# Optimization experiments

Measured on AMD Instinct MI355X. Metric: run time of the kernel, lower is better.

## Reference

```python
import jax, jax.numpy as jnp
import numpy as np

OUT, IN, GROUP = 11008, 4096, 64
NUM_GROUPS = IN // GROUP  # pad = 0 since IN % GROUP == 0


def setup_inputs() -> dict:
    key = jax.random.key(0)
    k_x, k_q, k_s, k_b = jax.random.split(key, 4)
    x = jax.random.normal(k_x, (4, 2048, IN), dtype=jnp.float32)
    # int4 symmetric codes in [-8, 7], stored as int8 like the torch buffer
    qweight = jax.random.randint(k_q, (OUT, NUM_GROUPS, GROUP), -8, 8).astype(jnp.int8)
    # positive per-group scales (amax/7 in the original), stored fp16
    scales = (jax.random.uniform(k_s, (OUT, NUM_GROUPS), dtype=jnp.float32) * 0.02 + 1e-3).astype(jnp.float16)
    bias = (jax.random.normal(k_b, (OUT,), dtype=jnp.float32) * 0.02).astype(jnp.float16)
    return {"x": x, "qweight": qweight, "scales": scales, "bias": bias}


def reference(x, qweight, scales, bias):
    # Fused dequant: w[o, g*GROUP + j] = q[o, g, j] * scales[o, g]
    w = (qweight.astype(jnp.float16) * scales[:, :, None]).reshape(OUT, IN)
    w = w.astype(x.dtype)  # original casts dequantized weight to x.dtype
    # F.linear(x, w, bias): y = x @ w.T + b  -> [B, S, OUT]
    return jnp.einsum('bsi,oi->bso', x, w) + bias.astype(x.dtype)
```

## Files before the change

kernel.cpp:

```cpp
#include <hip/hip_runtime.h>
#include <hip/hip_fp16.h>
#include <stdint.h>


#define M_DIM 8192
#define N_DIM 11008
#define K_DIM 4096
#define MT_TILES 64
#define NT_TILES 43
#define K_TILES 128
#define SLAB 8192
#define RSTRIDE 12288

typedef short short8 __attribute__((ext_vector_type(8)));
typedef float floatx4 __attribute__((ext_vector_type(4)));

__device__ __forceinline__ unsigned short f2bf(float f) {
  union { float f; uint32_t u; } c; c.f = f;
  uint32_t u = c.u;
  return (unsigned short)((u + 0x7FFFu + ((u >> 16) & 1u)) >> 16);
}

__device__ __forceinline__ float load_sc(const void* p, size_t idx, bool is_f32) {
  if (is_f32) return ((const float*)p)[idx];
  return __half2float(((const __half*)p)[idx]);
}

__device__ __forceinline__ bool sniff_q_is_i32(const void* qv) {
  const int* w = (const int*)qv;
  bool ok = true;
  #pragma unroll
  for (int j = 0; j < 16; ++j) {
    int v = w[j];
    ok = ok && (v == (int)(signed char)(v & 0xFF));
  }
  return ok;
}
__device__ __forceinline__ bool sniff_s_is_f32(const void* sv) {
  const float* f = (const float*)sv;
  bool ok = true;
  #pragma unroll
  for (int j = 0; j < 8; ++j) {
    float v = f[j];
    ok = ok && (v > 4e-4f) && (v < 6e-2f);
  }
  return ok;
}

__device__ __forceinline__ void gload_lds16(const short* g, short* l) {
  __builtin_amdgcn_global_load_lds(
      (const __attribute__((address_space(1))) uint32_t*)g,
      (__attribute__((address_space(3))) uint32_t*)l, 16, 0, 0);
}

__global__ __launch_bounds__(256)
void prep_fused(const float* __restrict__ x, const void* __restrict__ qv,
                const void* __restrict__ sv,
                short* __restrict__ xh, short* __restrict__ wq) {
  const int tid = threadIdx.x;
  int b = blockIdx.x;

  if (b < NT_TILES * 256) {
    const bool q_is_i32 = sniff_q_is_i32(qv);
    const bool s_is_f32 = sniff_s_is_f32(sv);
    const int nt = b >> 8;
    const int rem = b & 255;
    const int kt = rem >> 1, half = rem & 1;
    const int r = half * 128 + (tid >> 1);
    const int s0 = (tid & 1) * 2;
    const int o = nt * 256 + r;
    const int k0 = kt * 32 + s0 * 8;

    const float s = load_sc(sv, (size_t)o * 64 + (kt >> 1), s_is_f32);

    int codes[16];
    if (q_is_i32) {
      const int* qq = (const int*)qv + (size_t)o * K_DIM + k0;
      #pragma unroll
      for (int j = 0; j < 4; ++j) {
        int4 t = ((const int4*)qq)[j];
        codes[j*4+0]=t.x; codes[j*4+1]=t.y; codes[j*4+2]=t.z; codes[j*4+3]=t.w;
      }
    } else {
      union { int4 v; int8_t c[16]; } u;
      u.v = *(const int4*)((const int8_t*)qv + (size_t)o * K_DIM + k0);
      #pragma unroll
      for (int j = 0; j < 16; ++j) codes[j] = (int)u.c[j];
    }

    short8 h0, h1;
    #pragma unroll
    for (int j = 0; j < 8; ++j) h0[j] = f2bf((float)codes[j] * s);
    #pragma unroll
    for (int j = 0; j < 8; ++j) h1[j] = f2bf((float)codes[8 + j] * s);

    const int w = (r >> 1) & 3;
    short* slab = wq + ((size_t)nt * K_TILES + kt) * SLAB;
    *(short8*)&slab[r * 32 + ((s0    ) ^ w) * 8] = h0;
    *(short8*)&slab[r * 32 + ((s0 + 1) ^ w) * 8] = h1;
  } else {
    b -= NT_TILES * 256;
    const int mt = b >> 8;
    const int rem = b & 255;
    const int kt = rem >> 1, half = rem & 1;
    const int r = half * 128 + (tid >> 1);
    const int s0 = (tid & 1) * 2;
    const int k0 = kt * 32 + s0 * 8;

    const float4* p = (const float4*)(x + (size_t)(mt * 256 + r) * K_DIM + k0);
    float4 f0 = p[0], f1 = p[1], f2 = p[2], f3 = p[3];
    short8 h0, h1;
    h0[0]=f2bf(f0.x); h0[1]=f2bf(f0.y); h0[2]=f2bf(f0.z); h0[3]=f2bf(f0.w);
    h0[4]=f2bf(f1.x); h0[5]=f2bf(f1.y); h0[6]=f2bf(f1.z); h0[7]=f2bf(f1.w);
    h1[0]=f2bf(f2.x); h1[1]=f2bf(f2.y); h1[2]=f2bf(f2.z); h1[3]=f2bf(f2.w);
    h1[4]=f2bf(f3.x); h1[5]=f2bf(f3.y); h1[6]=f2bf(f3.z); h1[7]=f2bf(f3.w);

    const int w = (r >> 1) & 3;
    short* slab = xh + ((size_t)mt * K_TILES + kt) * SLAB;
    *(short8*)&slab[r * 32 + ((s0    ) ^ w) * 8] = h0;
    *(short8*)&slab[r * 32 + ((s0 + 1) ^ w) * 8] = h1;
  }
}

__global__ __launch_bounds__(256, 2)
void gemm4(const short* __restrict__ xh, const short* __restrict__ wq,
           const void* __restrict__ sv, const void* __restrict__ bv,
           float* __restrict__ C) {
  __shared__ __align__(16) short lds[3 * RSTRIDE];

  const bool s_is_f32 = sniff_s_is_f32(sv);

  const int tid  = threadIdx.x;
  const int lane = tid & 63;
  const int wid  = tid >> 6;
  const int wm = wid >> 1, wn = wid & 1;
  const int lr = lane & 15, lk = lane >> 4;

  const int bid = blockIdx.x;
  const int xcd = bid & 7;
  const int seq = bid >> 3;
  const int nt  = seq >> 3;
  const int mt  = xcd * 8 + (seq & 7);

  const short* Aslab = xh + (size_t)(mt >> 1) * (K_TILES * SLAB) + (mt & 1) * 4096;
  const short* Bslab = wq + (size_t)nt * (K_TILES * SLAB);

  const int swz8 = (lk ^ ((lr >> 1) & 3)) << 3;
  int aoff[4], boff[8];
  #pragma unroll
  for (int mi = 0; mi < 4; ++mi) aoff[mi] = (wm * 64 + mi * 16 + lr) * 32 + swz8;
  #pragma unroll
  for (int ni = 0; ni < 8; ++ni) boff[ni] = (wn * 128 + ni * 16 + lr) * 32 + swz8;

  floatx4 acc[4][8];
  #pragma unroll
  for (int i = 0; i < 4; ++i)
    #pragma unroll
    for (int j = 0; j < 8; ++j)
      acc[i][j] = (floatx4){0.f, 0.f, 0.f, 0.f};

  short8 fa[4], fb[8], ga[4], gb[8];

#define SBAR __builtin_amdgcn_sched_barrier(0)
#define VMCNT(n) do { asm volatile("s_waitcnt vmcnt(" #n ")"); SBAR; } while (0)
#define LGKM0 do { asm volatile("s_waitcnt lgkmcnt(0)"); SBAR; } while (0)
#define BARRIER do { SBAR; __builtin_amdgcn_s_barrier(); SBAR; } while (0)

#define STAGE(t) do {                                                   \
    const int s_ = (t) % 3;                                             \
    const short* gA_ = Aslab + (size_t)(t) * SLAB;                      \
    const short* gB_ = Bslab + (size_t)(t) * SLAB;                      \
    short* lA_ = lds + s_ * RSTRIDE;                                    \
    short* lB_ = lA_ + 4096;                                            \
    gload_lds16(gA_ + tid * 8,        lA_ + tid * 8);                   \
    gload_lds16(gA_ + 2048 + tid * 8, lA_ + 2048 + tid * 8);            \
    gload_lds16(gB_ + tid * 8,        lB_ + tid * 8);                   \
    gload_lds16(gB_ + 2048 + tid * 8, lB_ + 2048 + tid * 8);            \
    gload_lds16(gB_ + 4096 + tid * 8, lB_ + 4096 + tid * 8);            \
    gload_lds16(gB_ + 6144 + tid * 8, lB_ + 6144 + tid * 8);            \
  } while (0)

#define LOADF(da, db, t) do {                                           \
    const short* lA_ = lds + ((t) % 3) * RSTRIDE;                       \
    const short* lB_ = lA_ + 4096;                                      \
    _Pragma("unroll")                                                   \
    for (int mi = 0; mi < 4; ++mi) da[mi] = *(const short8*)&lA_[aoff[mi]]; \
    _Pragma("unroll")                                                   \
    for (int ni = 0; ni < 8; ++ni) db[ni] = *(const short8*)&lB_[boff[ni]]; \
  } while (0)

#define DOMFMA(sa, sb) do {                                             \
    __builtin_amdgcn_s_setprio(1);                                      \
    _Pragma("unroll")                                                   \
    for (int mi = 0; mi < 4; ++mi)                                      \
      _Pragma("unroll")                                                 \
      for (int ni = 0; ni < 8; ++ni)                                    \
        acc[mi][ni] = __builtin_amdgcn_mfma_f32_16x16x32_bf16(          \
            sa[mi], sb[ni], acc[mi][ni], 0, 0, 0);                      \
    __builtin_amdgcn_s_setprio(0);                                      \
  } while (0)

  STAGE(0); STAGE(1); STAGE(2);
  VMCNT(12);
  BARRIER;
  LOADF(fa, fb, 0);

  for (int kt = 0; kt < 124; kt += 2) {
    VMCNT(6);
    LGKM0;
    BARRIER;
    STAGE(kt + 3);
    LOADF(ga, gb, kt + 1);
    DOMFMA(fa, fb);
    VMCNT(6);
    LGKM0;
    BARRIER;
    STAGE(kt + 4);
    LOADF(fa, fb, kt + 2);
    DOMFMA(ga, gb);
  }

  VMCNT(6);
  LGKM0;
  BARRIER;
  STAGE(127);
  LOADF(ga, gb, 125);
  DOMFMA(fa, fb);
  VMCNT(6);
  LGKM0;
  BARRIER;
  LOADF(fa, fb, 126);
  DOMFMA(ga, gb);
  VMCNT(0);
  LGKM0;
  BARRIER;
  LOADF(ga, gb, 127);
  DOMFMA(fa, fb);
  DOMFMA(ga, gb);

#undef STAGE
#undef LOADF
#undef DOMFMA
#undef SBAR
#undef VMCNT
#undef LGKM0
#undef BARRIER

  #pragma unroll
  for (int ni = 0; ni < 8; ++ni) {
    const int col = nt * 256 + wn * 128 + ni * 16 + lr;
    const float bvf = load_sc(bv, (size_t)col, s_is_f32);
    #pragma unroll
    for (int mi = 0; mi < 4; ++mi) {
      const int rbase = mt * 128 + wm * 64 + mi * 16 + lk * 4;
      #pragma unroll
      for (int rr = 0; rr < 4; ++rr)
        C[(size_t)(rbase + rr) * N_DIM + col] = acc[mi][ni][rr] + bvf;
    }
  }
}

__global__ __launch_bounds__(256)
void gemm_fused(const float* __restrict__ x, const void* __restrict__ qv,
                const void* __restrict__ sv, const void* __restrict__ bv,
                float* __restrict__ C) {
  __shared__ __align__(16) short As[128 * 64];
  __shared__ __align__(16) short Bs[128 * 64];

  const bool q_is_i32 = sniff_q_is_i32(qv);
  const bool s_is_f32 = sniff_s_is_f32(sv);

  const int tid  = threadIdx.x;
  const int lane = tid & 63;
  const int wid  = tid >> 6;
  const int wm = wid >> 1, wn = wid & 1;
  const int lr = lane & 15, lk = lane >> 4;

  const int nwg = gridDim.x;
  const int cpx = nwg >> 3;
  const int bid = blockIdx.x;
  const int swz = (bid & 7) * cpx + (bid >> 3);
  const int per_g = 4 * 86;
  const int g = swz / per_g;
  const int r = swz - g * per_g;
  const int mt = (g << 2) + (r & 3);
  const int nt = r >> 2;

  const int row0 = mt * 128;
  const int col0 = nt * 128;

  floatx4 acc[4][4];
  #pragma unroll
  for (int i = 0; i < 4; ++i)
    #pragma unroll
    for (int j = 0; j < 4; ++j)
      acc[i][j] = (floatx4){0.f, 0.f, 0.f, 0.f};

  for (int kt = 0; kt < K_DIM / 64; ++kt) {
    const int k0 = kt * 64;
    #pragma unroll
    for (int i = 0; i < 4; ++i) {
      const int cid = i * 256 + tid;
      const int arow = cid >> 3, ac = (cid & 7) << 3;
      const float4* p = (const float4*)(x + (size_t)(row0 + arow) * K_DIM + k0 + ac);
      float4 a = p[0], b = p[1];
      short8 h;
      h[0]=f2bf(a.x); h[1]=f2bf(a.y); h[2]=f2bf(a.z); h[3]=f2bf(a.w);
      h[4]=f2bf(b.x); h[5]=f2bf(b.y); h[6]=f2bf(b.z); h[7]=f2bf(b.w);
      *(short8*)&As[arow * 64 + ac] = h;
    }
    #pragma unroll
    for (int i = 0; i < 2; ++i) {
      const int cid = i * 256 + tid;
      const int brow = cid >> 2, bc = (cid & 3) << 4;
      const float s = load_sc(sv, (size_t)(col0 + brow) * 64 + kt, s_is_f32);
      int codes[16];
      if (q_is_i32) {
        const int* qq = (const int*)qv + (size_t)(col0 + brow) * K_DIM + k0 + bc;
        #pragma unroll
        for (int j = 0; j < 4; ++j) {
          int4 t = ((const int4*)qq)[j];
          codes[j*4+0]=t.x; codes[j*4+1]=t.y; codes[j*4+2]=t.z; codes[j*4+3]=t.w;
        }
      } else {
        union { int4 v; int8_t c[16]; } u;
        u.v = *(const int4*)((const int8_t*)qv + (size_t)(col0 + brow) * K_DIM + k0 + bc);
        #pragma unroll
        for (int j = 0; j < 16; ++j) codes[j] = (int)u.c[j];
      }
      short8 h0, h1;
      #pragma unroll
      for (int j = 0; j < 8; ++j) h0[j] = f2bf((float)codes[j] * s);
      #pragma unroll
      for (int j = 0; j < 8; ++j) h1[j] = f2bf((float)codes[8 + j] * s);
      *(short8*)&Bs[brow * 64 + bc]     = h0;
      *(short8*)&Bs[brow * 64 + bc + 8] = h1;
    }
    __syncthreads();
    #pragma unroll
    for (int ks = 0; ks < 2; ++ks) {
      short8 a[4], b[4];
      #pragma unroll
      for (int mi = 0; mi < 4; ++mi)
        a[mi] = *(const short8*)&As[(wm * 64 + mi * 16 + lr) * 64 + ks * 32 + lk * 8];
      #pragma unroll
      for (int ni = 0; ni < 4; ++ni)
        b[ni] = *(const short8*)&Bs[(wn * 64 + ni * 16 + lr) * 64 + ks * 32 + lk * 8];
      #pragma unroll
      for (int mi = 0; mi < 4; ++mi)
        #pragma unroll
        for (int ni = 0; ni < 4; ++ni)
          acc[mi][ni] = __builtin_amdgcn_mfma_f32_16x16x32_bf16(
              a[mi], b[ni], acc[mi][ni], 0, 0, 0);
    }
    __syncthreads();
  }

  #pragma unroll
  for (int ni = 0; ni < 4; ++ni) {
    const int col = col0 + wn * 64 + ni * 16 + lr;
    const float bvf = load_sc(bv, (size_t)col, s_is_f32);
    #pragma unroll
    for (int mi = 0; mi < 4; ++mi) {
      const int rbase = row0 + wm * 64 + mi * 16 + lk * 4;
      #pragma unroll
      for (int rr = 0; rr < 4; ++rr)
        C[(size_t)(rbase + rr) * N_DIM + col] = acc[mi][ni][rr] + bvf;
    }
  }
}

extern "C" void kernel_launch(void* const* d_in, const int* in_sizes, int n_in,
                              void* d_out, int out_size, void* d_ws, size_t ws_size,
                              hipStream_t stream) {
  const float* x  = (const float*)d_in[0];
  const void*  q  = (const void*)d_in[1];
  const void*  sc = (const void*)d_in[2];
  const void*  bs = (const void*)d_in[3];
  float* y = (float*)d_out;
  (void)in_sizes; (void)n_in; (void)out_size;

  const size_t xh_bytes = (size_t)M_DIM * K_DIM * 2;
  const size_t wq_bytes = (size_t)N_DIM * K_DIM * 2;

  if (ws_size >= xh_bytes + wq_bytes) {
    short* xh = (short*)d_ws;
    short* wq = (short*)((char*)d_ws + xh_bytes);
    prep_fused<<<NT_TILES * 256 + (M_DIM / 256) * 256, dim3(256), 0, stream>>>(
        x, q, sc, xh, wq);
    gemm4<<<MT_TILES * NT_TILES, dim3(256), 0, stream>>>(xh, wq, sc, bs, y);
  } else {
    gemm_fused<<<(M_DIM / 128) * (N_DIM / 128), dim3(256), 0, stream>>>(x, q, sc, bs, y);
  }
}
```

Measured before the change: 751.4 us.

## Switch GEMM to 32x32x16 bf16 MFMA with matching fragment-major slab layout

Replaces the 16x16x32 MFMA tiling with 32x32x16 MFMAs, giving each warp a 2x4 grid of 32x32 accumulators. The prepack kernels now write A and B slabs in a lane-contiguous fragment order, so each LDS fragment read is a linear 16-byte-per-lane load and the XOR swizzle is no longer needed. The aim is fewer MFMA issues and fewer LDS reads per k-step, plus higher MFMA throughput per instruction. The epilogue is rewritten for the 32x32 accumulator row mapping, and bank-conflict behaviour now depends on the new linear layout.

New measurement: 798.5 us. +6.3%, slower.

```diff
diff --git a/kernel.cpp b/kernel.cpp
--- a/kernel.cpp
+++ b/kernel.cpp
@@ -9,11 +9,12 @@
 #define MT_TILES 64
 #define NT_TILES 43
 #define K_TILES 128
-#define SLAB 8192
+#define ASLAB 4096
+#define BSLAB 8192
 #define RSTRIDE 12288
 
 typedef short short8 __attribute__((ext_vector_type(8)));
-typedef float floatx4 __attribute__((ext_vector_type(4)));
+typedef float floatx16 __attribute__((ext_vector_type(16)));
 
 __device__ __forceinline__ unsigned short f2bf(float f) {
   union { float f; uint32_t u; } c; c.f = f;
@@ -94,20 +95,22 @@
     #pragma unroll
     for (int j = 0; j < 8; ++j) h1[j] = f2bf((float)codes[8 + j] * s);
 
-    const int w = (r >> 1) & 3;
-    short* slab = wq + ((size_t)nt * K_TILES + kt) * SLAB;
-    *(short8*)&slab[r * 32 + ((s0    ) ^ w) * 8] = h0;
-    *(short8*)&slab[r * 32 + ((s0 + 1) ^ w) * 8] = h1;
+    short* slab = wq + ((size_t)nt * K_TILES + kt) * BSLAB;
+    const int cb = r >> 5, rl = r & 31;
+    *(short8*)&slab[cb * 1024 + (s0 >> 1) * 512 + rl * 8]        = h0;
+    *(short8*)&slab[cb * 1024 + (s0 >> 1) * 512 + (rl + 32) * 8] = h1;
   } else {
     b -= NT_TILES * 256;
-    const int mt = b >> 8;
+    const int mtt = b >> 8;
     const int rem = b & 255;
     const int kt = rem >> 1, half = rem & 1;
-    const int r = half * 128 + (tid >> 1);
+    const int r256 = half * 128 + (tid >> 1);
     const int s0 = (tid & 1) * 2;
+    const int m = mtt * 256 + r256;
+    const int mt = m >> 7, r = m & 127;
     const int k0 = kt * 32 + s0 * 8;
 
-    const float4* p = (const float4*)(x + (size_t)(mt * 256 + r) * K_DIM + k0);
+    const float4* p = (const float4*)(x + (size_t)m * K_DIM + k0);
     float4 f0 = p[0], f1 = p[1], f2 = p[2], f3 = p[3];
     short8 h0, h1;
     h0[0]=f2bf(f0.x); h0[1]=f2bf(f0.y); h0[2]=f2bf(f0.z); h0[3]=f2bf(f0.w);
@@ -115,10 +118,10 @@
     h1[0]=f2bf(f2.x); h1[1]=f2bf(f2.y); h1[2]=f2bf(f2.z); h1[3]=f2bf(f2.w);
     h1[4]=f2bf(f3.x); h1[5]=f2bf(f3.y); h1[6]=f2bf(f3.z); h1[7]=f2bf(f3.w);
 
-    const int w = (r >> 1) & 3;
-    short* slab = xh + ((size_t)mt * K_TILES + kt) * SLAB;
-    *(short8*)&slab[r * 32 + ((s0    ) ^ w) * 8] = h0;
-    *(short8*)&slab[r * 32 + ((s0 + 1) ^ w) * 8] = h1;
+    short* slab = xh + ((size_t)mt * K_TILES + kt) * ASLAB;
+    const int rb = r >> 5, rl = r & 31;
+    *(short8*)&slab[rb * 1024 + (s0 >> 1) * 512 + rl * 8]        = h0;
+    *(short8*)&slab[rb * 1024 + (s0 >> 1) * 512 + (rl + 32) * 8] = h1;
   }
 }
 
@@ -134,7 +137,7 @@
   const int lane = tid & 63;
   const int wid  = tid >> 6;
   const int wm = wid >> 1, wn = wid & 1;
-  const int lr = lane & 15, lk = lane >> 4;
+  const int l31 = lane & 31, l5 = lane >> 5;
 
   const int bid = blockIdx.x;
   const int xcd = bid & 7;
@@ -142,24 +145,28 @@
   const int nt  = seq >> 3;
   const int mt  = xcd * 8 + (seq & 7);
 
-  const short* Aslab = xh + (size_t)(mt >> 1) * (K_TILES * SLAB) + (mt & 1) * 4096;
-  const short* Bslab = wq + (size_t)nt * (K_TILES * SLAB);
-
-  const int swz8 = (lk ^ ((lr >> 1) & 3)) << 3;
-  int aoff[4], boff[8];
-  #pragma unroll
-  for (int mi = 0; mi < 4; ++mi) aoff[mi] = (wm * 64 + mi * 16 + lr) * 32 + swz8;
-  #pragma unroll
-  for (int ni = 0; ni < 8; ++ni) boff[ni] = (wn * 128 + ni * 16 + lr) * 32 + swz8;
-
-  floatx4 acc[4][8];
-  #pragma unroll
-  for (int i = 0; i < 4; ++i)
-    #pragma unroll
-    for (int j = 0; j < 8; ++j)
-      acc[i][j] = (floatx4){0.f, 0.f, 0.f, 0.f};
-
-  short8 fa[4], fb[8], ga[4], gb[8];
+  const short* Aslab = xh + (size_t)mt * (K_TILES * ASLAB);
+  const short* Bslab = wq + (size_t)nt * (K_TILES * BSLAB);
+
+  int aoff[2][2], boff[2][4];
+  #pragma unroll
+  for (int kh = 0; kh < 2; ++kh) {
+    #pragma unroll
+    for (int ma = 0; ma < 2; ++ma)
+      aoff[kh][ma] = ((wm * 2 + ma) * 2 + kh) * 512 + lane * 8;
+    #pragma unroll
+    for (int nb = 0; nb < 4; ++nb)
+      boff[kh][nb] = ((wn * 4 + nb) * 2 + kh) * 512 + lane * 8;
+  }
+
+  floatx16 acc[2][4];
+  #pragma unroll
+  for (int i = 0; i < 2; ++i)
+    #pragma unroll
+    for (int j = 0; j < 4; ++j)
+      acc[i][j] = (floatx16)(0.f);
+
+  short8 fa[2][2], fb[2][4], ga[2][2], gb[2][4];
 
 #define SBAR __builtin_amdgcn_sched_barrier(0)
 #define VMCNT(n) do { asm volatile("s_waitcnt vmcnt(" #n ")"); SBAR; } while (0)
@@ -168,10 +175,10 @@
 
 #define STAGE(t) do {                                                   \
     const int s_ = (t) % 3;                                             \
-    const short* gA_ = Aslab + (size_t)(t) * SLAB;                      \
-    const short* gB_ = Bslab + (size_t)(t) * SLAB;                      \
+    const short* gA_ = Aslab + (size_t)(t) * ASLAB;                     \
+    const short* gB_ = Bslab + (size_t)(t) * BSLAB;                     \
     short* lA_ = lds + s_ * RSTRIDE;                                    \
-    short* lB_ = lA_ + 4096;                                            \
+    short* lB_ = lA_ + ASLAB;                                           \
     gload_lds16(gA_ + tid * 8,        lA_ + tid * 8);                   \
     gload_lds16(gA_ + 2048 + tid * 8, lA_ + 2048 + tid * 8);            \
     gload_lds16(gB_ + tid * 8,        lB_ + tid * 8);                   \
@@ -182,21 +189,28 @@
 
 #define LOADF(da, db, t) do {                                           \
     const short* lA_ = lds + ((t) % 3) * RSTRIDE;                       \
-    const short* lB_ = lA_ + 4096;                                      \
+    const short* lB_ = lA_ + ASLAB;                                     \
     _Pragma("unroll")                                                   \
-    for (int mi = 0; mi < 4; ++mi) da[mi] = *(const short8*)&lA_[aoff[mi]]; \
-    _Pragma("unroll")                                                   \
-    for (int ni = 0; ni < 8; ++ni) db[ni] = *(const short8*)&lB_[boff[ni]]; \
+    for (int kh = 0; kh < 2; ++kh) {                                    \
+      _Pragma("unroll")                                                 \
+      for (int ma = 0; ma < 2; ++ma)                                    \
+        da[kh][ma] = *(const short8*)&lA_[aoff[kh][ma]];                \
+      _Pragma("unroll")                                                 \
+      for (int nb = 0; nb < 4; ++nb)                                    \
+        db[kh][nb] = *(const short8*)&lB_[boff[kh][nb]];                \
+    }                                                                   \
   } while (0)
 
 #define DOMFMA(sa, sb) do {                                             \
     __builtin_amdgcn_s_setprio(1);                                      \
     _Pragma("unroll")                                                   \
-    for (int mi = 0; mi < 4; ++mi)                                      \
+    for (int kh = 0; kh < 2; ++kh)                                      \
       _Pragma("unroll")                                                 \
-      for (int ni = 0; ni < 8; ++ni)                                    \
-        acc[mi][ni] = __builtin_amdgcn_mfma_f32_16x16x32_bf16(          \
-            sa[mi], sb[ni], acc[mi][ni], 0, 0, 0);                      \
+      for (int ma = 0; ma < 2; ++ma)                                    \
+        _Pragma("unroll")                                               \
+        for (int nb = 0; nb < 4; ++nb)                                  \
+          acc[ma][nb] = __builtin_amdgcn_mfma_f32_32x32x16_bf16(        \
+              sa[kh][ma], sb[kh][nb], acc[ma][nb], 0, 0, 0);            \
     __builtin_amdgcn_s_setprio(0);                                      \
   } while (0)
 
@@ -247,15 +261,17 @@
 #undef BARRIER
 
   #pragma unroll
-  for (int ni = 0; ni < 8; ++ni) {
-    const int col = nt * 256 + wn * 128 + ni * 16 + lr;
+  for (int nb = 0; nb < 4; ++nb) {
+    const int col = nt * 256 + wn * 128 + nb * 32 + l31;
     const float bvf = load_sc(bv, (size_t)col, s_is_f32);
     #pragma unroll
-    for (int mi = 0; mi < 4; ++mi) {
-      const int rbase = mt * 128 + wm * 64 + mi * 16 + lk * 4;
-      #pragma unroll
-      for (int rr = 0; rr < 4; ++rr)
-        C[(size_t)(rbase + rr) * N_DIM + col] = acc[mi][ni][rr] + bvf;
+    for (int ma = 0; ma < 2; ++ma) {
+      const int rbase = mt * 128 + wm * 64 + ma * 32 + l5 * 4;
+      #pragma unroll
+      for (int L = 0; L < 16; ++L) {
+        const int row = rbase + (L & 3) + 8 * (L >> 2);
+        C[(size_t)row * N_DIM + col] = acc[ma][nb][L] + bvf;
+      }
     }
   }
 }
@@ -266,6 +282,7 @@
                 float* __restrict__ C) {
   __shared__ __align__(16) short As[128 * 64];
   __shared__ __align__(16) short Bs[128 * 64];
+  typedef float floatx4 __attribute__((ext_vector_type(4)));
 
   const bool q_is_i32 = sniff_q_is_i32(qv);
   const bool s_is_f32 = sniff_s_is_f32(sv);
```
